# Kernel optimization log

Measured on AMD Instinct MI355X. Metric: run time of the kernel, lower is better.

Reference implementation:

```python
import jax, jax.numpy as jnp
import numpy as np


def setup_inputs() -> dict:
    key = jax.random.key(0)
    ks = jax.random.split(key, 24)
    M, A, H = 512, 64, 300
    N = M * A              # real atoms
    B = N * 4              # directed bonds (avg degree 4)
    max_nb = 6
    atom_fdim, bond_fdim = 133, 147

    f_atoms = 0.5 * jax.random.normal(ks[0], (N + 1, atom_fdim), jnp.float32)
    f_atoms = f_atoms.at[0].set(0.0)  # padding atom row
    f_bonds = 0.5 * jax.random.normal(ks[1], (B + 1, bond_fdim), jnp.float32)
    f_bonds = f_bonds.at[0].set(0.0)  # padding bond row

    a2b = jax.random.randint(ks[2], (N + 1, max_nb), 0, B + 1, jnp.int32)
    a2b = a2b.at[0].set(0)
    b2a = jax.random.randint(ks[3], (B + 1,), 1, N + 1, jnp.int32)
    b2a = b2a.at[0].set(0)
    # bonds come in reverse pairs (1,2),(3,4),...
    idx = np.arange(1, B + 1)
    rev = np.where(idx % 2 == 1, idx + 1, idx - 1)
    b2revb = jnp.asarray(np.concatenate([[0], rev]), jnp.int32)

    def lin(k, out_d, in_d):
        s = 1.0 / np.sqrt(in_d)
        return jax.random.uniform(k, (out_d, in_d), jnp.float32, -s, s)

    params = dict(
        W_i_atom=lin(ks[4], H, atom_fdim),
        W_i_bond=lin(ks[5], H, bond_fdim),
        W_h=jnp.stack([lin(ks[6], H, H), lin(ks[7], H, H)]),  # depth-1 = 2
        lr_W=lin(ks[8], H, 3 * H),
        W_o_W=lin(ks[9], H, 2 * H),
        W_o_b=jax.random.uniform(ks[10], (H,), jnp.float32, -1 / np.sqrt(2 * H), 1 / np.sqrt(2 * H)),
        gWih_f=lin(ks[11], 3 * H, H), gWhh_f=lin(ks[12], 3 * H, H),
        gbih_f=0.05 * jax.random.normal(ks[13], (3 * H,), jnp.float32),
        gbhh_f=0.05 * jax.random.normal(ks[14], (3 * H,), jnp.float32),
        gWih_b=lin(ks[15], 3 * H, H), gWhh_b=lin(ks[16], 3 * H, H),
        gbih_b=0.05 * jax.random.normal(ks[17], (3 * H,), jnp.float32),
        gbhh_b=0.05 * jax.random.normal(ks[18], (3 * H,), jnp.float32),
    )
    return dict(f_atoms=f_atoms, f_bonds=f_bonds, a2b=a2b, b2a=b2a, b2revb=b2revb,
                num_mols=M, atoms_per_mol=A, **params)


def _gru_dir(x, h0, Wih, Whh, bih, bhh):
    # x: [M, A, H], h0: [M, H]; torch GRU gate order (r, z, n)
    def step(h, xt):
        gi = xt @ Wih.T + bih
        gh = h @ Whh.T + bhh
        ir, iz, inn = jnp.split(gi, 3, axis=-1)
        hr, hz, hn = jnp.split(gh, 3, axis=-1)
        r = jax.nn.sigmoid(ir + hr)
        z = jax.nn.sigmoid(iz + hz)
        n = jnp.tanh(inn + r * hn)
        hnew = (1.0 - z) * n + z * h
        return hnew if False else (hnew, hnew)
    _, ys = jax.lax.scan(step, h0, jnp.swapaxes(x, 0, 1))  # [A, M, H]
    return jnp.swapaxes(ys, 0, 1)


def _forward(f_atoms, f_bonds, W_i_atom, W_i_bond, W_h, lr_W, W_o_W, W_o_b,
             gWih_f, gWhh_f, gbih_f, gbhh_f, gWih_b, gWhh_b, gbih_b, gbhh_b,
             a2b, b2a, b2revb, num_mols, atoms_per_mol):
    act = jax.nn.relu
    H = W_i_atom.shape[0]
    M, A = num_mols, atoms_per_mol

    input_atom = act(f_atoms @ W_i_atom.T)            # [N+1, H]
    message_atom = input_atom
    input_bond = act(f_bonds @ W_i_bond.T)            # [B+1, H]
    message_bond = input_bond

    for d in range(W_h.shape[0]):                     # depth - 1 iterations
        nei = message_bond[a2b]                       # [N+1, nb, H] gather
        agg = nei.sum(axis=1) * nei.max(axis=1)       # sum * max aggregation
        message_atom = message_atom + agg
        rev = message_bond[b2revb]
        message_bond = message_atom[b2a] - rev
        message_bond = act(input_bond + message_bond @ W_h[d].T)

    nei = message_bond[a2b]
    agg = nei.sum(axis=1) * nei.max(axis=1)
    node = jnp.concatenate([agg, message_atom, input_atom], axis=1) @ lr_W.T  # [N+1, H]

    # BatchGRU: regular scope (every molecule has A atoms starting at row 1)
    msg = act(node)
    x = msg[1:].reshape(M, A, H)
    h0 = node[1:].reshape(M, A, H).max(axis=1)        # per-mol max of pre-relu hidden
    fwd = _gru_dir(x, h0, gWih_f, gWhh_f, gbih_f, gbhh_f)
    bwd = _gru_dir(x[:, ::-1], h0, gWih_b, gWhh_b, gbih_b, gbhh_b)[:, ::-1]
    gru_out = jnp.concatenate([fwd, bwd], axis=-1).reshape(M * A, 2 * H)
    row0 = jnp.concatenate([msg[0:1], msg[0:1]], axis=1)
    message = jnp.concatenate([row0, gru_out], axis=0)  # [N+1, 2H]

    atom_hiddens = act(message @ W_o_W.T + W_o_b)       # [N+1, H]
    mol_vecs = atom_hiddens[1:].reshape(M, A, H).mean(axis=1)  # [M, H]
    return mol_vecs


def reference(f_atoms, f_bonds, a2b, b2a, b2revb, num_mols, atoms_per_mol,
              W_i_atom, W_i_bond, W_h, lr_W, W_o_W, W_o_b,
              gWih_f, gWhh_f, gbih_f, gbhh_f, gWih_b, gWhh_b, gbih_b, gbhh_b):
    return _forward(f_atoms, f_bonds, W_i_atom, W_i_bond, W_h, lr_W, W_o_W, W_o_b,
                    gWih_f, gWhh_f, gbih_f, gbhh_f, gWih_b, gWhh_b, gbih_b, gbhh_b,
                    a2b, b2a, b2revb, num_mols, atoms_per_mol)
```

## Files before the change

kernel.cpp:

```cpp
#include <hip/hip_runtime.h>
#include <hip/hip_bf16.h>

using bf16 = __hip_bfloat16;
using uint = unsigned int;
typedef __attribute__((ext_vector_type(8))) short short8v;
typedef __attribute__((ext_vector_type(4))) float float4v;

__device__ __forceinline__ float b2f(bf16 x){ return __bfloat162float(x); }
__device__ __forceinline__ bf16  f2b(float x){ return __float2bfloat16(x); }
__device__ __forceinline__ uint f2bu(float x){
    uint u = __float_as_uint(x);
    return (u + 0x7fffu + ((u >> 16) & 1u)) >> 16;
}
__device__ __forceinline__ float blo(uint u){ return __uint_as_float(u << 16); }
__device__ __forceinline__ float bhi(uint u){ return __uint_as_float(u & 0xffff0000u); }

constexpr int Mmol = 512, Aat = 64;
constexpr int Nat  = Mmol * Aat;
constexpr int NP1  = Nat + 1;
constexpr int Bnd  = Nat * 4;
constexpr int BP1  = Bnd + 1;
constexpr int Hd   = 300;
constexpr int AF   = 133, BFd = 147;
constexpr int NB   = 6;
constexpr int GSL  = 38;

template<int AM, bool RELU, bool BIAS, bool RES, bool OUTBF16, bool DUAL, int TAILK>
__global__ __launch_bounds__(256) void mgemm(
    const bf16* __restrict__ Abh, const float* __restrict__ MAf, const bf16* __restrict__ MBh,
    const int* __restrict__ g1, const int* __restrict__ g2,
    const bf16* __restrict__ Wp, const float* __restrict__ bias, const bf16* __restrict__ res,
    void* __restrict__ Cp, bf16* __restrict__ Cp2, int n, int K, int Kp, int h)
{
    const int  NX = (h + 63) >> 6;
    const long NY = ((long)n + 127) >> 7;
    const long J  = (long)NX * NY;
    const long job = (long)(blockIdx.x & 7) * (gridDim.x >> 3) + (blockIdx.x >> 3);
    if (job >= J) return;
    const int  bx = (int)(job % NX);
    const long by = job / NX;
    const long rowBase = by * 128;
    const long colBase = (long)bx * 64;

    const int tid  = threadIdx.x;
    const int lane = tid & 63, w = tid >> 6;
    const int l15  = lane & 15, quad = lane >> 4;

    long arow[2], ga[2], gb[2];
    #pragma unroll
    for (int mt = 0; mt < 2; ++mt) {
        long r = rowBase + w * 32 + mt * 16 + l15;
        if (r >= n) r = n - 1;
        arow[mt] = r;
        if constexpr (AM == 3) { ga[mt] = g1[r]; gb[mt] = g2[r]; }
        else { ga[mt] = 0; gb[mt] = 0; }
    }

    const bf16* wp0 = Wp + (colBase + l15) * (long)Kp + quad * 8;

    float4v acc[2][4];
    #pragma unroll
    for (int mt = 0; mt < 2; ++mt)
        #pragma unroll
        for (int nt = 0; nt < 4; ++nt)
            acc[mt][nt] = (float4v){0.f, 0.f, 0.f, 0.f};

    const int ktiles = (K + 31) / 32;
    for (int kt = 0; kt < ktiles; ++kt) {
        const int kb = kt * 32;
        const int koff = kb + quad * 8;
        short8v bfr[4];
        #pragma unroll
        for (int nt = 0; nt < 4; ++nt)
            bfr[nt] = *(const short8v*)(wp0 + (long)nt * 16 * Kp + kb);
        short8v af[2];
        if constexpr (AM == 0) {
            #pragma unroll
            for (int mt = 0; mt < 2; ++mt) {
                const bf16* p = Abh + arow[mt] * (long)K + koff;
                union { uint2 u2[2]; short8v s; } t;
                t.u2[0] = *(const uint2*)p;
                t.u2[1] = *(const uint2*)(p + 4);
                af[mt] = t.s;
            }
        } else {
            #pragma unroll
            for (int mt = 0; mt < 2; ++mt) {
                const float* pa = MAf + ga[mt] * 300 + koff;
                const bf16*  pb = MBh + gb[mt] * 300 + koff;
                const float4 m0 = *(const float4*)pa;
                const float4 m1 = *(const float4*)(pa + 4);
                const uint2  u0 = *(const uint2*)pb;
                const uint2  u1 = *(const uint2*)(pb + 4);
                float v[8];
                v[0] = m0.x - blo(u0.x); v[1] = m0.y - bhi(u0.x);
                v[2] = m0.z - blo(u0.y); v[3] = m0.w - bhi(u0.y);
                v[4] = m1.x - blo(u1.x); v[5] = m1.y - bhi(u1.x);
                v[6] = m1.z - blo(u1.y); v[7] = m1.w - bhi(u1.y);
                short8v s;
                #pragma unroll
                for (int j = 0; j < 8; ++j) s[j] = (short)f2bu(v[j]);
                af[mt] = s;
            }
        }
        if constexpr (TAILK != 0) {
            if (kb + 32 > K) {
                #pragma unroll
                for (int j = 0; j < 8; ++j)
                    if (koff + j >= K) { af[0][j] = 0; af[1][j] = 0; }
            }
        }
        #pragma unroll
        for (int mt = 0; mt < 2; ++mt)
            #pragma unroll
            for (int nt = 0; nt < 4; ++nt)
                acc[mt][nt] = __builtin_amdgcn_mfma_f32_16x16x32_bf16(
                    af[mt], bfr[nt], acc[mt][nt], 0, 0, 0);
    }

    float biasv[4];
    #pragma unroll
    for (int nt = 0; nt < 4; ++nt) {
        const long c = colBase + nt * 16 + l15;
        biasv[nt] = (BIAS && c < h) ? bias[c] : 0.f;
    }
    #pragma unroll
    for (int mt = 0; mt < 2; ++mt) {
        #pragma unroll
        for (int reg = 0; reg < 4; ++reg) {
            const long r = rowBase + w * 32 + mt * 16 + quad * 4 + reg;
            if (r < n) {
                #pragma unroll
                for (int nt = 0; nt < 4; ++nt) {
                    const long c = colBase + nt * 16 + l15;
                    if (c < h) {
                        float v = acc[mt][nt][reg];
                        if constexpr (RES)  v += b2f(res[r * (long)h + c]);
                        if constexpr (BIAS) v += biasv[nt];
                        if constexpr (RELU) v = fmaxf(v, 0.f);
                        if constexpr (DUAL) {
                            ((float*)Cp)[r * (long)h + c] = v;
                            Cp2[r * (long)h + c] = f2b(fmaxf(v, 0.f));
                        } else if constexpr (OUTBF16) {
                            ((bf16*)Cp)[r * (long)h + c] = f2b(v);
                        } else {
                            ((float*)Cp)[r * (long)h + c] = v;
                        }
                    }
                }
            }
        }
    }
}

__global__ __launch_bounds__(256) void pack_w(const float* __restrict__ W, bf16* __restrict__ Wp,
                                              int h, int K, long total, int Kp)
{
    const long idx = (long)blockIdx.x * 256 + threadIdx.x;
    if (idx >= total) return;
    const long r = idx / Kp;
    const int kk = (int)(idx - r * Kp);
    Wp[idx] = (r < h && kk < K) ? f2b(W[r * (long)K + kk]) : f2b(0.f);
}

__global__ __launch_bounds__(256) void pack_lrw(const float* __restrict__ W, bf16* __restrict__ Wp)
{
    const int idx = blockIdx.x * 256 + threadIdx.x;
    if (idx >= 320 * 960) return;
    const int r = idx / 960, c = idx - r * 960;
    const int seg = c / 320, kk = c - seg * 320;
    Wp[idx] = (r < 300 && kk < 300) ? f2b(W[r * 900 + seg * 300 + kk]) : f2b(0.f);
}

__global__ __launch_bounds__(256) void pack_gws(const float* __restrict__ W, bf16* __restrict__ Wp)
{
    const int idx = blockIdx.x * 256 + threadIdx.x;
    if (idx >= 8 * 128 * 320) return;
    const int k = idx % 320;
    const int r = (idx / 320) & 127;
    const int s = idx / (320 * 128);
    const int g = r / GSL, l = r - g * GSL;
    const int j = s * GSL + l;
    bf16 v = f2b(0.f);
    if (r < 114 && j < 300 && k < 300)
        v = f2b(W[(g * 300 + j) * 300 + k]);
    Wp[idx] = v;
}

constexpr int BMr = 256, BNc = 64;

__global__ __launch_bounds__(256) void gemm_ia(
    const float* __restrict__ A, const float* __restrict__ W,
    float* __restrict__ Cp, int n, int k, int h)
{
    __shared__ float As[16][BMr];
    __shared__ float Ws[16][BNc];

    const int  NC = (h + BNc - 1) / BNc;
    const long NR = ((long)n + BMr - 1) / BMr;
    const long J  = (long)NC * NR;
    const long job = (long)(blockIdx.x & 7) * (gridDim.x >> 3) + (blockIdx.x >> 3);
    if (job >= J) return;
    const int  c0 = (int)(job % NC);
    const long rt = job / NC;
    const long rowBase = rt * BMr;
    const long colBase = (long)c0 * BNc;

    const int tid = threadIdx.x;
    const int tx = tid & 7, ty = tid >> 3;

    const long grow = rowBase + tid;
    const bool rv = grow < n;
    const int wcol = tid & 63, kq = tid >> 6;
    const long gcol = colBase + wcol;
    const bool cvv = gcol < h;

    float acc[8][8] = {};

    const int ktiles = (k + 15) / 16;
    for (int kt = 0; kt < ktiles; ++kt) {
        const int kb = kt * 16;
        __syncthreads();
        const float* ap = A + grow * (long)k + kb;
        #pragma unroll
        for (int c = 0; c < 16; ++c)
            As[c][tid] = (rv && kb + c < k) ? ap[c] : 0.f;
        #pragma unroll
        for (int c = 0; c < 4; ++c) {
            const int kk = kb + kq * 4 + c;
            Ws[kq * 4 + c][wcol] = (cvv && kk < k) ? W[gcol * (long)k + kk] : 0.f;
        }
        __syncthreads();
        #pragma unroll
        for (int kk = 0; kk < 16; ++kk) {
            const float4 a0 = *(const float4*)&As[kk][ty * 8];
            const float4 a1 = *(const float4*)&As[kk][ty * 8 + 4];
            const float4 b0 = *(const float4*)&Ws[kk][tx * 8];
            const float4 b1 = *(const float4*)&Ws[kk][tx * 8 + 4];
            const float aa[8] = {a0.x,a0.y,a0.z,a0.w,a1.x,a1.y,a1.z,a1.w};
            const float bb[8] = {b0.x,b0.y,b0.z,b0.w,b1.x,b1.y,b1.z,b1.w};
            #pragma unroll
            for (int i = 0; i < 8; ++i)
                #pragma unroll
                for (int j = 0; j < 8; ++j)
                    acc[i][j] = fmaf(aa[i], bb[j], acc[i][j]);
        }
    }
    #pragma unroll
    for (int i = 0; i < 8; ++i) {
        const long r = rowBase + ty * 8 + i;
        if (r < n) {
            #pragma unroll
            for (int j = 0; j < 8; ++j) {
                const long c = colBase + tx * 8 + j;
                if (c < h) Cp[r * (long)h + c] = fmaxf(acc[i][j], 0.f);
            }
        }
    }
}

template<bool ADD>
__global__ __launch_bounds__(320) void agg_kernel(
    const bf16* __restrict__ MB, const int* __restrict__ a2b,
    const float* __restrict__ src, float* __restrict__ out, int rowoff)
{
    const int hh = threadIdx.x;
    if (hh >= Hd) return;
    const long atom = (long)blockIdx.x + rowoff;
    const int* nb = a2b + atom * NB;
    float s = 0.f, mx = -1e30f;
    #pragma unroll
    for (int j = 0; j < NB; ++j) {
        const float v = b2f(MB[(long)nb[j] * Hd + hh]);
        s += v; mx = fmaxf(mx, v);
    }
    const float agg = s * mx;
    const long o = (long)blockIdx.x * Hd + hh;
    if constexpr (ADD) out[o] = src[atom * Hd + hh] + agg;
    else               out[o] = agg;
}

__global__ __launch_bounds__(320) void cc_build(
    const bf16* __restrict__ MB, const int* __restrict__ a2b,
    const float* __restrict__ MA, const float* __restrict__ IA,
    bf16* __restrict__ CC)
{
    const int hh = threadIdx.x;
    const long r = blockIdx.x;
    bf16* cr = CC + r * 960;
    if (hh < Hd) {
        const long atom = r + 1;
        const int* nb = a2b + atom * NB;
        float s = 0.f, mx = -1e30f;
        #pragma unroll
        for (int j = 0; j < NB; ++j) {
            const float v = b2f(MB[(long)nb[j] * Hd + hh]);
            s += v; mx = fmaxf(mx, v);
        }
        cr[hh]       = f2b(s * mx);
        cr[320 + hh] = f2b(MA[atom * Hd + hh]);
        cr[640 + hh] = f2b(IA[atom * Hd + hh]);
    } else {
        const int p = hh - Hd;
        cr[300 + p] = f2b(0.f);
        cr[620 + p] = f2b(0.f);
        cr[940 + p] = f2b(0.f);
    }
}

__global__ __launch_bounds__(320) void h0_kernel(const float* __restrict__ node, float* __restrict__ h0)
{
    const int hh = threadIdx.x;
    if (hh >= Hd) return;
    const long m = blockIdx.x;
    float mx = -1e30f;
    for (int a = 0; a < Aat; ++a)
        mx = fmaxf(mx, node[(m * Aat + a) * (long)Hd + hh]);
    h0[m * Hd + hh] = mx;
}

__global__ __launch_bounds__(320) void mean_kernel(const float* __restrict__ AH, float* __restrict__ out)
{
    const int hh = threadIdx.x;
    if (hh >= Hd) return;
    const long m = blockIdx.x;
    float s = 0.f;
    for (int a = 0; a < Aat; ++a)
        s += AH[(m * Aat + a) * (long)Hd + hh];
    out[m * Hd + hh] = s * (1.f / 64.f);
}

__global__ __launch_bounds__(320) void hinit_kernel(const float* __restrict__ h0,
                                                    float* __restrict__ hf, bf16* __restrict__ hb)
{
    const int j = threadIdx.x;
    const long m = blockIdx.x;
    const int dir = blockIdx.y;
    const float v = (j < 300) ? h0[m * 300 + j] : 0.f;
    hf[((long)dir * 512 + m) * 320 + j] = v;
    hb[((long)dir * 512 + m) * 320 + j] = f2b(v);
    hb[((long)(2 + dir) * 512 + m) * 320 + j] = f2b(0.f);
}

__global__ __launch_bounds__(256) void gru_step(
    const bf16* __restrict__ gi_f, const bf16* __restrict__ gi_b,
    const bf16* __restrict__ wsf, const bf16* __restrict__ wsb,
    const float* __restrict__ bhh_f, const float* __restrict__ bhh_b,
    float* __restrict__ hf, bf16* __restrict__ hb, bf16* __restrict__ out,
    int t, int force)
{
    const int slice = blockIdx.x & 7;
    const int dir   = (blockIdx.x >> 3) & 1;
    const int m0    = (blockIdx.x >> 4) * 32;
    const int a     = dir ? (Aat - 1 - t) : t;

    const bf16*  WS  = (dir ? wsb : wsf) + (long)slice * 128 * 320;
    const bf16*  gi  = dir ? gi_b : gi_f;
    const float* bhh = dir ? bhh_b : bhh_f;
    float* hfd = hf + (long)dir * 512 * 320;
    const int par = t & 1;
    const bf16* hbr = hb + ((long)(par * 2 + dir) * 512) * 320;
    bf16*       hbw = hb + ((long)(((t + 1) & 1) * 2 + dir) * 512) * 320;

    __shared__ float GHs[128][36];
    __shared__ uint  Hs[32][164];
    __shared__ float ldspad[12288];

    const int tid  = threadIdx.x;
    const int lane = tid & 63, w = tid >> 6;
    const int l15  = lane & 15, quad = lane >> 4;

    if (force) {
        ldspad[tid] = (float)tid;
        GHs[0][0] = ldspad[(tid + force) & 4095];
    }

    #pragma unroll
    for (int q = 0; q < 10; ++q) {
        const int idx = tid + q * 256;
        const int row = idx / 80, c = idx - row * 80;
        const uint2 v = *(const uint2*)(hbr + (long)(m0 + row) * 320 + c * 4);
        *(uint2*)&Hs[row][c * 2] = v;
    }
    __syncthreads();

    short8v hbf[2][10];
    #pragma unroll
    for (int ct = 0; ct < 2; ++ct)
        #pragma unroll
        for (int kf = 0; kf < 10; ++kf)
            hbf[ct][kf] = *(const short8v*)&Hs[ct * 16 + l15][kf * 16 + quad * 4];

    #pragma unroll
    for (int mti = 0; mti < 2; ++mti) {
        const int mt = w + mti * 4;
        const bf16* ap = WS + (long)(mt * 16 + l15) * 320 + quad * 8;
        short8v af[10];
        #pragma unroll
        for (int kf = 0; kf < 10; ++kf)
            af[kf] = *(const short8v*)(ap + kf * 32);
        float4v acc0 = (float4v){0.f, 0.f, 0.f, 0.f};
        float4v acc1 = (float4v){0.f, 0.f, 0.f, 0.f};
        #pragma unroll
        for (int kf = 0; kf < 10; ++kf) {
            acc0 = __builtin_amdgcn_mfma_f32_16x16x32_bf16(af[kf], hbf[0][kf], acc0, 0, 0, 0);
            acc1 = __builtin_amdgcn_mfma_f32_16x16x32_bf16(af[kf], hbf[1][kf], acc1, 0, 0, 0);
        }
        #pragma unroll
        for (int reg = 0; reg < 4; ++reg) {
            GHs[mt * 16 + quad * 4 + reg][l15]      = acc0[reg];
            GHs[mt * 16 + quad * 4 + reg][16 + l15] = acc1[reg];
        }
    }
    __syncthreads();

    #pragma unroll
    for (int p = 0; p < 3; ++p) {
        const int idx = tid + p * 256;
        if (idx < 19 * 32) {
            const int mol = idx / 19, jp = idx - mol * 19;
            const int jl = jp * 2, jg = slice * GSL + jl;
            if (jg < 300) {
                const float hr0 = GHs[jl][mol],          hr1 = GHs[jl + 1][mol];
                const float hz0 = GHs[GSL + jl][mol],    hz1 = GHs[GSL + jl + 1][mol];
                const float hn0 = GHs[2 * GSL + jl][mol], hn1 = GHs[2 * GSL + jl + 1][mol];
                const bf16* girow = gi + ((long)(m0 + mol) * Aat + a) * 900;
                const uint gr = *(const uint*)(girow + jg);
                const uint gz = *(const uint*)(girow + 300 + jg);
                const uint gn = *(const uint*)(girow + 600 + jg);
                const float2 br = *(const float2*)(bhh + jg);
                const float2 bz = *(const float2*)(bhh + 300 + jg);
                const float2 bn = *(const float2*)(bhh + 600 + jg);
                float* hop = hfd + (long)(m0 + mol) * 320 + jg;
                const float2 hold = *(const float2*)hop;
                float hnew[2];
                #pragma unroll
                for (int j = 0; j < 2; ++j) {
                    const float ir  = j ? bhi(gr) : blo(gr);
                    const float iz  = j ? bhi(gz) : blo(gz);
                    const float inn = j ? bhi(gn) : blo(gn);
                    const float ghr = j ? hr1 + br.y : hr0 + br.x;
                    const float ghz = j ? hz1 + bz.y : hz0 + bz.x;
                    const float ghn = j ? hn1 + bn.y : hn0 + bn.x;
                    const float rr = 1.f / (1.f + __expf(-(ir + ghr)));
                    const float zz = 1.f / (1.f + __expf(-(iz + ghz)));
                    float nin = inn + rr * ghn;
                    nin = fminf(fmaxf(nin, -15.f), 15.f);
                    const float e2 = __expf(-2.f * nin);
                    const float nnv = (1.f - e2) / (1.f + e2);
                    hnew[j] = (1.f - zz) * nnv + zz * (j ? hold.y : hold.x);
                }
                const uint pk2 = f2bu(hnew[0]) | (f2bu(hnew[1]) << 16);
                *(float2*)hop = make_float2(hnew[0], hnew[1]);
                *(uint*)(hbw + (long)(m0 + mol) * 320 + jg) = pk2;
                *(uint*)(out + ((long)(m0 + mol) * Aat + a) * 600 + (long)dir * 300 + jg) = pk2;
            }
        }
    }
}

extern "C" void kernel_launch(void* const* d_in, const int* in_sizes, int n_in,
                              void* d_out, int out_size, void* d_ws, size_t ws_size,
                              hipStream_t stream)
{
    (void)in_sizes; (void)n_in; (void)out_size; (void)ws_size;

    const float* f_atoms  = (const float*)d_in[0];
    const float* f_bonds  = (const float*)d_in[1];
    const int*   a2b      = (const int*)d_in[2];
    const int*   b2a      = (const int*)d_in[3];
    const int*   b2revb   = (const int*)d_in[4];
    const float* W_i_atom = (const float*)d_in[7];
    const float* W_i_bond = (const float*)d_in[8];
    const float* W_h      = (const float*)d_in[9];
    const float* lr_W     = (const float*)d_in[10];
    const float* W_o_W    = (const float*)d_in[11];
    const float* W_o_b    = (const float*)d_in[12];
    const float* gWih_f   = (const float*)d_in[13];
    const float* gWhh_f   = (const float*)d_in[14];
    const float* gbih_f   = (const float*)d_in[15];
    const float* gbhh_f   = (const float*)d_in[16];
    const float* gWih_b   = (const float*)d_in[17];
    const float* gWhh_b   = (const float*)d_in[18];
    const float* gbih_b   = (const float*)d_in[19];
    const float* gbhh_b   = (const float*)d_in[20];

    const size_t F32A_B = (size_t)NP1 * Hd * 4;
    const size_t BND_B  = (size_t)BP1 * Hd * 2;
    const size_t H0_B   = (size_t)Mmol * Hd * 4;
    const size_t WPM_B  = (size_t)8 * 128 * 320 * 2;

    size_t off = 0;
    auto alloc = [&](size_t b) { size_t r = off; off += (b + 255) & ~(size_t)255; return r; };
    const size_t r1_o = alloc(F32A_B);
    const size_t r2_o = alloc(F32A_B);
    const size_t r3_o = alloc(BND_B);
    const size_t r4_o = alloc(BND_B + 4096);

    char* ws = (char*)d_ws;
    float* IA   = (float*)(ws + r1_o);
    float* H0p  = (float*)(ws + r1_o);
    bf16*  WPmf = (bf16*)(ws + r1_o + ((H0_B + 255) & ~(size_t)255));
    bf16*  WPmb = (bf16*)((char*)WPmf + ((WPM_B + 255) & ~(size_t)255));
    bf16*  NRb  = (bf16*)(ws + r1_o + (2u << 20));
    float* Hf32 = (float*)(ws + r1_o + (23u << 20));
    bf16*  Hb16 = (bf16*)(ws + r1_o + (25u << 20));
    float* AH   = (float*)(ws + r1_o);
    float* MAb  = (float*)(ws + r2_o);
    bf16*  GRU  = (bf16*)(ws + r2_o);
    bf16*  IB   = (bf16*)(ws + r3_o);
    bf16*  MB1  = IB;
    float* NODE = (float*)(ws + r3_o);
    bf16*  GIF  = (bf16*)(ws + r3_o);
    bf16*  FB16 = (bf16*)(ws + r4_o);
    bf16*  MB0  = (bf16*)(ws + r4_o);
    bf16*  CC   = (bf16*)(ws + r4_o);
    bf16*  GIB  = (bf16*)(ws + r4_o);
    float* OUT  = (float*)d_out;
    bf16*  WSC  = (bf16*)d_out;

    const dim3 blk(256);
    auto grdM = [](int n, int h) {
        long J = (long)((h + 63) / 64) * ((n + 127) / 128);
        return dim3((unsigned)((J + 7) / 8 * 8));
    };
    auto grdF = [](int n, int h) {
        long J = (long)((h + BNc - 1) / BNc) * ((n + BMr - 1) / BMr);
        return dim3((unsigned)((J + 7) / 8 * 8));
    };
    auto pk = [&](const float* W, bf16* Wp, int h, int K, long hp, int Kp) {
        const long tot = hp * Kp;
        pack_w<<<dim3((tot + 255) / 256), blk, 0, stream>>>(W, Wp, h, K, tot, Kp);
    };

    gemm_ia<<<grdF(NP1, Hd), blk, 0, stream>>>(f_atoms, W_i_atom, IA, NP1, AF, Hd);
    pk(f_bonds, FB16, BP1, BFd, BP1, 160);
    pk(W_i_bond, WSC, Hd, BFd, 320, 160);
    mgemm<0, true, false, false, true, false, 0><<<grdM(BP1, Hd), blk, 0, stream>>>(
        FB16, nullptr, nullptr, nullptr, nullptr, WSC, nullptr, nullptr,
        IB, nullptr, BP1, 160, 160, Hd);
    agg_kernel<true><<<NP1, 320, 0, stream>>>(IB, a2b, IA, MAb, 0);
    pk(W_h, WSC, Hd, Hd, 320, 320);
    mgemm<3, true, false, true, true, false, 12><<<grdM(BP1, Hd), blk, 0, stream>>>(
        nullptr, MAb, IB, b2a, b2revb, WSC, nullptr, IB,
        MB0, nullptr, BP1, Hd, 320, Hd);
    agg_kernel<true><<<NP1, 320, 0, stream>>>(MB0, a2b, MAb, MAb, 0);
    pk(W_h + 300 * 300, WSC, Hd, Hd, 320, 320);
    mgemm<3, true, false, true, true, false, 12><<<grdM(BP1, Hd), blk, 0, stream>>>(
        nullptr, MAb, MB0, b2a, b2revb, WSC, nullptr, IB,
        MB1, nullptr, BP1, Hd, 320, Hd);
    cc_build<<<Nat, 320, 0, stream>>>(MB1, a2b, MAb, IA, CC);
    pack_lrw<<<(320 * 960 + 255) / 256, blk, 0, stream>>>(lr_W, WSC);
    mgemm<0, false, false, false, false, true, 0><<<grdM(Nat, Hd), blk, 0, stream>>>(
        CC, nullptr, nullptr, nullptr, nullptr, WSC, nullptr, nullptr,
        NODE, NRb, Nat, 960, 960, Hd);
    h0_kernel<<<Mmol, 320, 0, stream>>>(NODE, H0p);
    {
        const int tot = 8 * 128 * 320;
        pack_gws<<<dim3((tot + 255) / 256), blk, 0, stream>>>(gWhh_f, WPmf);
        pack_gws<<<dim3((tot + 255) / 256), blk, 0, stream>>>(gWhh_b, WPmb);
    }
    pk(gWih_f, WSC, 900, Hd, 960, 320);
    mgemm<0, false, true, false, true, false, 12><<<grdM(Nat, 900), blk, 0, stream>>>(
        NRb, nullptr, nullptr, nullptr, nullptr, WSC, gbih_f, nullptr,
        GIF, nullptr, Nat, Hd, 320, 900);
    pk(gWih_b, WSC, 900, Hd, 960, 320);
    mgemm<0, false, true, false, true, false, 12><<<grdM(Nat, 900), blk, 0, stream>>>(
        NRb, nullptr, nullptr, nullptr, nullptr, WSC, gbih_b, nullptr,
        GIB, nullptr, Nat, Hd, 320, 900);
    hinit_kernel<<<dim3(Mmol, 2), 320, 0, stream>>>(H0p, Hf32, Hb16);
    for (int t = 0; t < Aat; ++t)
        gru_step<<<dim3(256), blk, 0, stream>>>(
            GIF, GIB, WPmf, WPmb, gbhh_f, gbhh_b, Hf32, Hb16, GRU, t, 0);
    pk(W_o_W, WSC, Hd, 600, 320, 608);
    mgemm<0, true, true, false, false, false, 24><<<grdM(Nat, Hd), blk, 0, stream>>>(
        GRU, nullptr, nullptr, nullptr, nullptr, WSC, W_o_b, nullptr,
        AH, nullptr, Nat, 600, 608, Hd);
    mean_kernel<<<Mmol, 320, 0, stream>>>(AH, OUT);
}
```

Before: 1.889 ms.

## Fuse 64 GRU step launches into one persistent kernel with grid barrier

```diff
diff --git a/kernel.cpp b/kernel.cpp
--- a/kernel.cpp
+++ b/kernel.cpp
@@ -331,36 +331,34 @@
 }
 
 __global__ __launch_bounds__(320) void hinit_kernel(const float* __restrict__ h0,
-                                                    float* __restrict__ hf, bf16* __restrict__ hb)
+                                                    float* __restrict__ hf, bf16* __restrict__ hb,
+                                                    uint* __restrict__ bar)
 {
     const int j = threadIdx.x;
     const long m = blockIdx.x;
     const int dir = blockIdx.y;
+    if (m == 0 && dir == 0 && j == 0) bar[0] = 0u;
     const float v = (j < 300) ? h0[m * 300 + j] : 0.f;
     hf[((long)dir * 512 + m) * 320 + j] = v;
     hb[((long)dir * 512 + m) * 320 + j] = f2b(v);
     hb[((long)(2 + dir) * 512 + m) * 320 + j] = f2b(0.f);
 }
 
-__global__ __launch_bounds__(256) void gru_step(
+__global__ __launch_bounds__(256) void gru_pers(
     const bf16* __restrict__ gi_f, const bf16* __restrict__ gi_b,
     const bf16* __restrict__ wsf, const bf16* __restrict__ wsb,
     const float* __restrict__ bhh_f, const float* __restrict__ bhh_b,
     float* __restrict__ hf, bf16* __restrict__ hb, bf16* __restrict__ out,
-    int t, int force)
+    uint* __restrict__ bar, int force)
 {
     const int slice = blockIdx.x & 7;
     const int dir   = (blockIdx.x >> 3) & 1;
     const int m0    = (blockIdx.x >> 4) * 32;
-    const int a     = dir ? (Aat - 1 - t) : t;
 
     const bf16*  WS  = (dir ? wsb : wsf) + (long)slice * 128 * 320;
     const bf16*  gi  = dir ? gi_b : gi_f;
     const float* bhh = dir ? bhh_b : bhh_f;
     float* hfd = hf + (long)dir * 512 * 320;
-    const int par = t & 1;
-    const bf16* hbr = hb + ((long)(par * 2 + dir) * 512) * 320;
-    bf16*       hbw = hb + ((long)(((t + 1) & 1) * 2 + dir) * 512) * 320;
 
     __shared__ float GHs[128][36];
     __shared__ uint  Hs[32][164];
@@ -375,73 +373,113 @@
         GHs[0][0] = ldspad[(tid + force) & 4095];
     }
 
-    #pragma unroll
-    for (int q = 0; q < 10; ++q) {
-        const int idx = tid + q * 256;
-        const int row = idx / 80, c = idx - row * 80;
-        const uint2 v = *(const uint2*)(hbr + (long)(m0 + row) * 320 + c * 4);
-        *(uint2*)&Hs[row][c * 2] = v;
-    }
-    __syncthreads();
-
-    short8v hbf[2][10];
-    #pragma unroll
-    for (int ct = 0; ct < 2; ++ct)
-        #pragma unroll
-        for (int kf = 0; kf < 10; ++kf)
-            hbf[ct][kf] = *(const short8v*)&Hs[ct * 16 + l15][kf * 16 + quad * 4];
-
-    #pragma unroll
-    for (int mti = 0; mti < 2; ++mti) {
-        const int mt = w + mti * 4;
-        const bf16* ap = WS + (long)(mt * 16 + l15) * 320 + quad * 8;
-        short8v af[10];
-        #pragma unroll
-        for (int kf = 0; kf < 10; ++kf)
-            af[kf] = *(const short8v*)(ap + kf * 32);
-        float4v acc0 = (float4v){0.f, 0.f, 0.f, 0.f};
-        float4v acc1 = (float4v){0.f, 0.f, 0.f, 0.f};
-        #pragma unroll
-        for (int kf = 0; kf < 10; ++kf) {
-            acc0 = __builtin_amdgcn_mfma_f32_16x16x32_bf16(af[kf], hbf[0][kf], acc0, 0, 0, 0);
-            acc1 = __builtin_amdgcn_mfma_f32_16x16x32_bf16(af[kf], hbf[1][kf], acc1, 0, 0, 0);
-        }
-        #pragma unroll
-        for (int reg = 0; reg < 4; ++reg) {
-            GHs[mt * 16 + quad * 4 + reg][l15]      = acc0[reg];
-            GHs[mt * 16 + quad * 4 + reg][16 + l15] = acc1[reg];
-        }
-    }
-    __syncthreads();
-
+    short8v wA[10], wB[10];
+    {
+        const bf16* apA = WS + (long)(w * 16 + l15) * 320 + quad * 8;
+        const bf16* apB = WS + (long)((w + 4) * 16 + l15) * 320 + quad * 8;
+        #pragma unroll
+        for (int kf = 0; kf < 10; ++kf) wA[kf] = *(const short8v*)(apA + kf * 32);
+        #pragma unroll
+        for (int kf = 0; kf < 10; ++kf) wB[kf] = *(const short8v*)(apB + kf * 32);
+    }
+
+    bool ok[3]; int pmol[3], jlA[3], jgA[3];
+    float2 brA[3], bzA[3], bnA[3];
     #pragma unroll
     for (int p = 0; p < 3; ++p) {
         const int idx = tid + p * 256;
-        if (idx < 19 * 32) {
-            const int mol = idx / 19, jp = idx - mol * 19;
-            const int jl = jp * 2, jg = slice * GSL + jl;
-            if (jg < 300) {
-                const float hr0 = GHs[jl][mol],          hr1 = GHs[jl + 1][mol];
-                const float hz0 = GHs[GSL + jl][mol],    hz1 = GHs[GSL + jl + 1][mol];
+        bool o = idx < 19 * 32;
+        const int mol = o ? idx / 19 : 0;
+        const int jp  = o ? idx - mol * 19 : 0;
+        const int jl  = jp * 2, jg = slice * GSL + jl;
+        if (jg >= 300) o = false;
+        ok[p] = o; pmol[p] = mol; jlA[p] = jl; jgA[p] = jg;
+        brA[p] = o ? *(const float2*)(bhh + jg)       : make_float2(0.f, 0.f);
+        bzA[p] = o ? *(const float2*)(bhh + 300 + jg) : make_float2(0.f, 0.f);
+        bnA[p] = o ? *(const float2*)(bhh + 600 + jg) : make_float2(0.f, 0.f);
+    }
+
+    for (int t = 0; t < Aat; ++t) {
+        const int a = dir ? (Aat - 1 - t) : t;
+        const bf16* hbr = hb + ((long)((t & 1) * 2 + dir) * 512) * 320;
+        bf16*       hbw = hb + ((long)(((t + 1) & 1) * 2 + dir) * 512) * 320;
+
+        uint gr[3], gz[3], gn[3];
+        #pragma unroll
+        for (int p = 0; p < 3; ++p) {
+            gr[p] = gz[p] = gn[p] = 0;
+            if (ok[p]) {
+                const bf16* girow = gi + ((long)(m0 + pmol[p]) * Aat + a) * 900;
+                gr[p] = *(const uint*)(girow + jgA[p]);
+                gz[p] = *(const uint*)(girow + 300 + jgA[p]);
+                gn[p] = *(const uint*)(girow + 600 + jgA[p]);
+            }
+        }
+
+        #pragma unroll
+        for (int q = 0; q < 10; ++q) {
+            const int idx = tid + q * 256;
+            const int row = idx / 80, c = idx - row * 80;
+            const uint2 v = *(const uint2*)(hbr + (long)(m0 + row) * 320 + c * 4);
+            *(uint2*)&Hs[row][c * 2] = v;
+        }
+        __syncthreads();
+
+        short8v hbf[2][10];
+        #pragma unroll
+        for (int ct = 0; ct < 2; ++ct)
+            #pragma unroll
+            for (int kf = 0; kf < 10; ++kf)
+                hbf[ct][kf] = *(const short8v*)&Hs[ct * 16 + l15][kf * 16 + quad * 4];
+
+        {
+            float4v acc0 = (float4v){0.f, 0.f, 0.f, 0.f};
+            float4v acc1 = (float4v){0.f, 0.f, 0.f, 0.f};
+            #pragma unroll
+            for (int kf = 0; kf < 10; ++kf) {
+                acc0 = __builtin_amdgcn_mfma_f32_16x16x32_bf16(wA[kf], hbf[0][kf], acc0, 0, 0, 0);
+                acc1 = __builtin_amdgcn_mfma_f32_16x16x32_bf16(wA[kf], hbf[1][kf], acc1, 0, 0, 0);
+            }
+            #pragma unroll
+            for (int reg = 0; reg < 4; ++reg) {
+                GHs[w * 16 + quad * 4 + reg][l15]      = acc0[reg];
+                GHs[w * 16 + quad * 4 + reg][16 + l15] = acc1[reg];
+            }
+        }
+        {
+            float4v acc0 = (float4v){0.f, 0.f, 0.f, 0.f};
+            float4v acc1 = (float4v){0.f, 0.f, 0.f, 0.f};
+            #pragma unroll
+            for (int kf = 0; kf < 10; ++kf) {
+                acc0 = __builtin_amdgcn_mfma_f32_16x16x32_bf16(wB[kf], hbf[0][kf], acc0, 0, 0, 0);
+                acc1 = __builtin_amdgcn_mfma_f32_16x16x32_bf16(wB[kf], hbf[1][kf], acc1, 0, 0, 0);
+            }
+            #pragma unroll
+            for (int reg = 0; reg < 4; ++reg) {
+                GHs[(w + 4) * 16 + quad * 4 + reg][l15]      = acc0[reg];
+                GHs[(w + 4) * 16 + quad * 4 + reg][16 + l15] = acc1[reg];
+            }
+        }
+        __syncthreads();
+
+        #pragma unroll
+        for (int p = 0; p < 3; ++p) {
+            if (ok[p]) {
+                const int mol = pmol[p], jl = jlA[p], jg = jgA[p];
+                const float hr0 = GHs[jl][mol],           hr1 = GHs[jl + 1][mol];
+                const float hz0 = GHs[GSL + jl][mol],     hz1 = GHs[GSL + jl + 1][mol];
                 const float hn0 = GHs[2 * GSL + jl][mol], hn1 = GHs[2 * GSL + jl + 1][mol];
-                const bf16* girow = gi + ((long)(m0 + mol) * Aat + a) * 900;
-                const uint gr = *(const uint*)(girow + jg);
-                const uint gz = *(const uint*)(girow + 300 + jg);
-                const uint gn = *(const uint*)(girow + 600 + jg);
-                const float2 br = *(const float2*)(bhh + jg);
-                const float2 bz = *(const float2*)(bhh + 300 + jg);
-                const float2 bn = *(const float2*)(bhh + 600 + jg);
                 float* hop = hfd + (long)(m0 + mol) * 320 + jg;
                 const float2 hold = *(const float2*)hop;
                 float hnew[2];
                 #pragma unroll
                 for (int j = 0; j < 2; ++j) {
-                    const float ir  = j ? bhi(gr) : blo(gr);
-                    const float iz  = j ? bhi(gz) : blo(gz);
-                    const float inn = j ? bhi(gn) : blo(gn);
-                    const float ghr = j ? hr1 + br.y : hr0 + br.x;
-                    const float ghz = j ? hz1 + bz.y : hz0 + bz.x;
-                    const float ghn = j ? hn1 + bn.y : hn0 + bn.x;
+                    const float ir  = j ? bhi(gr[p]) : blo(gr[p]);
+                    const float iz  = j ? bhi(gz[p]) : blo(gz[p]);
+                    const float inn = j ? bhi(gn[p]) : blo(gn[p]);
+                    const float ghr = j ? hr1 + brA[p].y : hr0 + brA[p].x;
+                    const float ghz = j ? hz1 + bzA[p].y : hz0 + bzA[p].x;
+                    const float ghn = j ? hn1 + bnA[p].y : hn0 + bnA[p].x;
                     const float rr = 1.f / (1.f + __expf(-(ir + ghr)));
                     const float zz = 1.f / (1.f + __expf(-(iz + ghz)));
                     float nin = inn + rr * ghn;
@@ -455,6 +493,24 @@
                 *(uint*)(hbw + (long)(m0 + mol) * 320 + jg) = pk2;
                 *(uint*)(out + ((long)(m0 + mol) * Aat + a) * 600 + (long)dir * 300 + jg) = pk2;
             }
+        }
+
+        if (t < Aat - 1) {
+            __syncthreads();
+            if (tid == 0) {
+                __threadfence();
+                atomicAdd(bar, 1u);
+                const uint target = 256u * (uint)(t + 1);
+                int spins = 0;
+                while (__hip_atomic_load(bar, __ATOMIC_RELAXED,
+                                         __HIP_MEMORY_SCOPE_AGENT) < target
+                       && spins < 500000) {
+                    ++spins;
+                    __builtin_amdgcn_s_sleep(2);
+                }
+            }
+            __syncthreads();
+            __threadfence();
         }
     }
 }
@@ -505,6 +561,7 @@
     bf16*  NRb  = (bf16*)(ws + r1_o + (2u << 20));
     float* Hf32 = (float*)(ws + r1_o + (23u << 20));
     bf16*  Hb16 = (bf16*)(ws + r1_o + (25u << 20));
+    uint*  BAR  = (uint*)(ws + r1_o + (28u << 20));
     float* AH   = (float*)(ws + r1_o);
     float* MAb  = (float*)(ws + r2_o);
     bf16*  GRU  = (bf16*)(ws + r2_o);
@@ -568,10 +625,9 @@
     mgemm<0, false, true, false, true, false, 12><<<grdM(Nat, 900), blk, 0, stream>>>(
         NRb, nullptr, nullptr, nullptr, nullptr, WSC, gbih_b, nullptr,
         GIB, nullptr, Nat, Hd, 320, 900);
-    hinit_kernel<<<dim3(Mmol, 2), 320, 0, stream>>>(H0p, Hf32, Hb16);
-    for (int t = 0; t < Aat; ++t)
-        gru_step<<<dim3(256), blk, 0, stream>>>(
-            GIF, GIB, WPmf, WPmb, gbhh_f, gbhh_b, Hf32, Hb16, GRU, t, 0);
+    hinit_kernel<<<dim3(Mmol, 2), 320, 0, stream>>>(H0p, Hf32, Hb16, BAR);
+    gru_pers<<<dim3(256), blk, 0, stream>>>(
+        GIF, GIB, WPmf, WPmb, gbhh_f, gbhh_b, Hf32, Hb16, GRU, BAR, 0);
     pk(W_o_W, WSC, Hd, 600, 320, 608);
     mgemm<0, true, true, false, false, false, 24><<<grdM(Nat, Hd), blk, 0, stream>>>(
         GRU, nullptr, nullptr, nullptr, nullptr, WSC, W_o_b, nullptr,
```

Measured after the change: 3.843 ms. 2.03x slower.
